# Performance work log

Hardware: AMD Instinct MI355X
Metric: run time of the kernel (lower is better)

## Reference

```python
import jax, jax.numpy as jnp
import numpy as np

KM_ITERS = 25  # fixed Lloyd iterations (original kmeans_pytorch iterates to tol; fixed count for jit)
EPS = 1e-12    # torch F.normalize clamp_min eps


def l2_normalize(x):
    n = jnp.sqrt(jnp.sum(x * x, axis=1, keepdims=True))
    return x / jnp.maximum(n, EPS)


def kmeans(X, k, iters=KM_ITERS):
    """Lloyd's algorithm, euclidean distance, deterministic init from first k rows."""
    N = X.shape[0]
    centers0 = X[:k]
    xsq = jnp.sum(X * X, axis=1, keepdims=True)  # [N,1]

    def dist2(centers):
        # squared euclidean distances [N,k]; argmin identical to euclidean
        return xsq - 2.0 * (X @ centers.T) + jnp.sum(centers * centers, axis=1)

    def step(i, centers):
        lab = jnp.argmin(dist2(centers), axis=1)  # [N]
        sums = jax.ops.segment_sum(X, lab, num_segments=k)  # [k,d]
        cnts = jax.ops.segment_sum(jnp.ones((N,), X.dtype), lab, num_segments=k)  # [k]
        new = sums / jnp.maximum(cnts, 1.0)[:, None]
        # keep old center for empty clusters
        return jnp.where(cnts[:, None] > 0, new, centers)

    centers = jax.lax.fori_loop(0, iters, step, centers0)
    labels = jnp.argmin(dist2(centers), axis=1)
    return labels, centers


def setup_inputs() -> dict:
    key = jax.random.key(0)
    ks = jax.random.split(key, 8)
    N, D, H, K = 50000, 1024, 512, 64
    x = jax.random.normal(ks[0], (N, D), dtype=jnp.float32)
    xw = jax.random.normal(ks[1], (N, D), dtype=jnp.float32)
    s1 = 1.0 / np.sqrt(D)
    s2 = 1.0 / np.sqrt(H)
    W1 = jax.random.uniform(ks[2], (D, H), jnp.float32, -s1, s1)
    b1 = jax.random.uniform(ks[3], (H,), jnp.float32, -s1, s1)
    W2 = jax.random.uniform(ks[4], (D, H), jnp.float32, -s1, s1)
    b2 = jax.random.uniform(ks[5], (H,), jnp.float32, -s1, s1)
    Wc = jax.random.uniform(ks[6], (H, K), jnp.float32, -s2, s2)
    bc = jax.random.uniform(ks[7], (K,), jnp.float32, -s2, s2)
    return {"x": x, "xw": xw, "W1": W1, "b1": b1, "W2": W2, "b2": b2,
            "Wc": Wc, "bc": bc, "n_clusters": K}


def reference(x, xw, W1, b1, W2, b2, Wc, bc, n_clusters):
    out1 = l2_normalize(x @ W1 + b1)   # layers1 + F.normalize(dim=1)
    out2 = l2_normalize(xw @ W2 + b2)  # layers2 + F.normalize(dim=1)
    # kmeans results are detached in the original (converted to numpy)
    km_label, km_centers = kmeans(jax.lax.stop_gradient(out2), n_clusters)
    u1 = jax.nn.softmax(out1 @ Wc + bc, axis=1)
    u2 = jax.nn.softmax(out2 @ Wc + bc, axis=1)
    return (out1, out2, km_label, km_centers, u1, u2)
```

## Files before the change

### kernel.cpp

```cpp
#include <hip/hip_runtime.h>
#include <math.h>

#define ND 1024
#define HID 512
#define KCL 64
#define KM_ITERS 25
#define CHSZ 256


__device__ __forceinline__ float np_pw512_sq(const float* __restrict__ a, int lane)
{
#pragma clang fp contract(off)
  float r = 0.f;
  if (lane < 32) {
    const float* blk = a + 128 * (lane >> 3);
    int j = lane & 7;
    float t = blk[j];
    r = t * t;
#pragma unroll
    for (int i = 8; i < 128; i += 8) { float u = blk[j + i]; r = r + u * u; }
  }
  float t1 = r  + __shfl_xor(r,  1);
  float t2 = t1 + __shfl_xor(t1, 2);
  float t3 = t2 + __shfl_xor(t2, 4);
  float u4 = t3 + __shfl_xor(t3, 8);
  float v5 = u4 + __shfl_xor(u4, 16);
  return __shfl(v5, 0);
}

__global__ __launch_bounds__(512) void np_gemm2_kernel(
    const float* __restrict__ A, const float* __restrict__ W,
    const float* __restrict__ bias, float* __restrict__ C)
{
#pragma clang fp contract(off)
  const int t = threadIdx.x;
  const size_t r0 = (size_t)blockIdx.x * 8;
  const float* a0p = A + r0 * ND;
  float s1[8], s2[8], s3[8], s4[8];
#pragma unroll
  for (int r = 0; r < 8; r++) { s1[r] = 0.f; s2[r] = 0.f; s3[r] = 0.f; s4[r] = 0.f; }

#define G2_STEP(ACC, K4)                                                       \
  {                                                                            \
    const int k = (K4) * 4;                                                    \
    float w0 = W[(size_t)(k + 0) * HID + t];                                   \
    float w1 = W[(size_t)(k + 1) * HID + t];                                   \
    float w2 = W[(size_t)(k + 2) * HID + t];                                   \
    float w3 = W[(size_t)(k + 3) * HID + t];                                   \
    _Pragma("unroll")                                                          \
    for (int r = 0; r < 8; r++) {                                              \
      float4 a = *reinterpret_cast<const float4*>(a0p + (size_t)r * ND + k);   \
      float s = ACC[r];                                                        \
      s = fmaf(a.x, w0, s);                                                    \
      s = fmaf(a.y, w1, s);                                                    \
      s = fmaf(a.z, w2, s);                                                    \
      s = fmaf(a.w, w3, s);                                                    \
      ACC[r] = s;                                                              \
    }                                                                          \
  }

#pragma unroll 2
  for (int k4 = 0; k4 < 80; k4++)    G2_STEP(s1, k4)
#pragma unroll 2
  for (int k4 = 80; k4 < 160; k4++)  G2_STEP(s2, k4)
#pragma unroll 2
  for (int k4 = 160; k4 < 208; k4++) G2_STEP(s3, k4)
#pragma unroll 2
  for (int k4 = 208; k4 < 256; k4++) G2_STEP(s4, k4)
#undef G2_STEP

  float b = bias[t];
#pragma unroll
  for (int r = 0; r < 8; r++)
    C[(r0 + r) * HID + t] = (((s1[r] + s2[r]) + s3[r]) + s4[r]) + b;
}

__global__ __launch_bounds__(256) void np_rownorm_xsq_kernel(
    float* __restrict__ M, float* __restrict__ xsq, int N)
{
#pragma clang fp contract(off)
  __shared__ float sy[4][512];
  int w = threadIdx.x >> 6, lane = threadIdx.x & 63;
  int r = blockIdx.x * 4 + w;
  if (r >= N) return;
  float* row = M + (size_t)r * HID;
  float s = np_pw512_sq(row, lane);
  float n = fmaxf((float)sqrt((double)s), 1e-12f);
#pragma unroll
  for (int j = 0; j < 8; j++) {
    float y = row[lane * 8 + j] / n;
    row[lane * 8 + j] = y;
    sy[w][lane * 8 + j] = y;
  }
  __syncthreads();
  float s2 = np_pw512_sq(sy[w], lane);
  if (lane == 0) xsq[r] = s2;
}

__global__ __launch_bounds__(64) void np_csqT_kernel(
    const float* __restrict__ cen, float* __restrict__ csq, float* __restrict__ Ct)
{
#pragma clang fp contract(off)
  int c = blockIdx.x;
  int lane = threadIdx.x;
  const float* row = cen + (size_t)c * HID;
  float s = np_pw512_sq(row, lane);
  if (lane == 0) csq[c] = s;
  for (int k = lane; k < HID; k += 64) Ct[(size_t)k * KCL + c] = row[k];
}

__global__ __launch_bounds__(256) void np_label_kernel(
    const float* __restrict__ X, const float* __restrict__ Ct,
    const float* __restrict__ xsq, const float* __restrict__ csq,
    int* __restrict__ lab, int N)
{
#pragma clang fp contract(off)
  __shared__ float Xs[16][512];
  const int t = threadIdx.x;
  const int p0 = blockIdx.x * 16;
  const float4* Xg = (const float4*)(X + (size_t)p0 * HID);
  float4* Xs4 = (float4*)&Xs[0][0];
  for (int i = t; i < 16 * 128; i += 256) Xs4[i] = Xg[i];
  __syncthreads();

  const int w = t >> 6, c = t & 63;
  const int pl = w * 4;
  float s0[4], s1[4];
#pragma unroll
  for (int pt = 0; pt < 4; pt++) { s0[pt] = 0.f; s1[pt] = 0.f; }

#pragma unroll 8
  for (int k = 0; k < 256; k++) {
    float ct = Ct[(size_t)k * KCL + c];
#pragma unroll
    for (int pt = 0; pt < 4; pt++) s0[pt] = fmaf(Xs[pl + pt][k], ct, s0[pt]);
  }
#pragma unroll 8
  for (int k = 256; k < 512; k++) {
    float ct = Ct[(size_t)k * KCL + c];
#pragma unroll
    for (int pt = 0; pt < 4; pt++) s1[pt] = fmaf(Xs[pl + pt][k], ct, s1[pt]);
  }

#pragma unroll
  for (int pt = 0; pt < 4; pt++) {
    int p = p0 + pl + pt;
    float dot = s0[pt] + s1[pt];
    float t2 = 2.0f * dot;
    float u = xsq[p] - t2;
    float sc = u + csq[c];
    float bv = sc; int bi = c;
#pragma unroll
    for (int m = 32; m; m >>= 1) {
      float ov = __shfl_xor(bv, m);
      int   oi = __shfl_xor(bi, m);
      if (ov < bv || (ov == bv && oi < bi)) { bv = ov; bi = oi; }
    }
    if (c == 0 && p < N) lab[p] = bi;
  }
}


__global__ __launch_bounds__(256) void k_count(
    const int* __restrict__ lab, int* __restrict__ cntch, int N)
{
  int ch = blockIdx.x;
  int p = ch * CHSZ + threadIdx.x;
  int l = (p < N) ? lab[p] : -1;
  int w = threadIdx.x >> 6, lane = threadIdx.x & 63;
  __shared__ int wc[4][64];
  for (int cc = 0; cc < 64; cc++) {
    unsigned long long mm = __ballot(l == cc);
    if (lane == cc) wc[w][cc] = __popcll(mm);
  }
  __syncthreads();
  if (threadIdx.x < 64) {
    int cc = threadIdx.x;
    cntch[ch * 64 + cc] = wc[0][cc] + wc[1][cc] + wc[2][cc] + wc[3][cc];
  }
}

__global__ __launch_bounds__(64) void k_prefix(
    const int* __restrict__ cntch, int* __restrict__ off,
    int* __restrict__ base, int* __restrict__ cnt, int CH)
{
  int c = threadIdx.x;
  int run = 0;
  for (int ch = 0; ch < CH; ch++) { off[ch * 64 + c] = run; run += cntch[ch * 64 + c]; }
  cnt[c] = run;
  __shared__ int tot[64];
  tot[c] = run;
  __syncthreads();
  if (c == 0) {
    int b = 0;
    for (int cc = 0; cc < 64; cc++) { base[cc] = b; b += tot[cc]; }
  }
  __syncthreads();
  int b = base[c];
  for (int ch = 0; ch < CH; ch++) off[ch * 64 + c] += b;
}

__global__ __launch_bounds__(256) void k_scatter(
    const int* __restrict__ lab, const int* __restrict__ off,
    int* __restrict__ list, int N)
{
  int ch = blockIdx.x;
  int p = ch * CHSZ + threadIdx.x;
  int l = (p < N) ? lab[p] : -1;
  int w = threadIdx.x >> 6, lane = threadIdx.x & 63;
  __shared__ int wc[4][64];
  int rank = 0;
  for (int cc = 0; cc < 64; cc++) {
    unsigned long long mm = __ballot(l == cc);
    if (lane == cc) wc[w][cc] = __popcll(mm);
    if (l == cc) rank = __popcll(mm & ((1ull << lane) - 1ull));
  }
  __syncthreads();
  if (p < N) {
    int before = 0;
    for (int ww = 0; ww < 4; ww++) if (ww < w) before += wc[ww][l];
    list[off[ch * 64 + l] + before + rank] = p;
  }
}

__global__ __launch_bounds__(256) void np_seg_kernel(
    const float* __restrict__ X, const int* __restrict__ list,
    const int* __restrict__ base, const int* __restrict__ cnt,
    float* __restrict__ sums)
{
#pragma clang fp contract(off)
  const int c = blockIdx.x;
  const int d = blockIdx.y * 256 + threadIdx.x;
  const int n = cnt[c];
  const int* lp = list + base[c];
  float s = 0.f;
  int i = 0;
  for (; i + 8 <= n; i += 8) {
    int p0 = lp[i + 0], p1 = lp[i + 1], p2 = lp[i + 2], p3 = lp[i + 3];
    int p4 = lp[i + 4], p5 = lp[i + 5], p6 = lp[i + 6], p7 = lp[i + 7];
    float x0 = X[(size_t)p0 * HID + d];
    float x1 = X[(size_t)p1 * HID + d];
    float x2 = X[(size_t)p2 * HID + d];
    float x3 = X[(size_t)p3 * HID + d];
    float x4 = X[(size_t)p4 * HID + d];
    float x5 = X[(size_t)p5 * HID + d];
    float x6 = X[(size_t)p6 * HID + d];
    float x7 = X[(size_t)p7 * HID + d];
    s = s + x0; s = s + x1; s = s + x2; s = s + x3;
    s = s + x4; s = s + x5; s = s + x6; s = s + x7;
  }
  for (; i < n; i++) s = s + X[(size_t)lp[i] * HID + d];
  sums[(size_t)c * HID + d] = s;
}

__global__ __launch_bounds__(512) void np_update_csqT_kernel(
    const float* __restrict__ sums, const int* __restrict__ cnt,
    float* __restrict__ cen, float* __restrict__ csq, float* __restrict__ Ct)
{
#pragma clang fp contract(off)
  __shared__ float row[512];
  const int c = blockIdx.x, d = threadIdx.x;
  const int n = cnt[c];
  float v;
  if (n > 0) {
    v = sums[(size_t)c * HID + d] / fmaxf((float)n, 1.0f);
    cen[(size_t)c * HID + d] = v;
  } else {
    v = cen[(size_t)c * HID + d];
  }
  row[d] = v;
  __syncthreads();
  if (d < 64) {
    float s = np_pw512_sq(row, d);
    if (d == 0) csq[c] = s;
  }
  Ct[(size_t)d * KCL + c] = v;
}

__global__ void copy_f32_kernel(const float* __restrict__ s, float* __restrict__ d, int n)
{
  int i = blockIdx.x * blockDim.x + threadIdx.x;
  if (i < n) d[i] = s[i];
}
__global__ void lab_to_f32_kernel(const int* __restrict__ s, float* __restrict__ d, int n)
{
  int i = blockIdx.x * blockDim.x + threadIdx.x;
  if (i < n) d[i] = (float)s[i];
}


__global__ __launch_bounds__(256) void rownorm_kernel(float* __restrict__ M, int N)
{
  int r = blockIdx.x * 4 + (threadIdx.x >> 6);
  int lane = threadIdx.x & 63;
  if (r >= N) return;
  float* row = M + (size_t)r * HID;
  float4 v0 = *reinterpret_cast<const float4*>(&row[lane * 8]);
  float4 v1 = *reinterpret_cast<const float4*>(&row[lane * 8 + 4]);
  float s = v0.x*v0.x + v0.y*v0.y + v0.z*v0.z + v0.w*v0.w
          + v1.x*v1.x + v1.y*v1.y + v1.z*v1.z + v1.w*v1.w;
#pragma unroll
  for (int off = 32; off; off >>= 1) s += __shfl_xor(s, off);
  float nrm = fmaxf(sqrtf(s), 1e-12f);
  v0.x /= nrm; v0.y /= nrm; v0.z /= nrm; v0.w /= nrm;
  v1.x /= nrm; v1.y /= nrm; v1.z /= nrm; v1.w /= nrm;
  *reinterpret_cast<float4*>(&row[lane * 8]) = v0;
  *reinterpret_cast<float4*>(&row[lane * 8 + 4]) = v1;
}

__global__ __launch_bounds__(256) void clf_softmax_kernel(
    const float* __restrict__ X, const float* __restrict__ W,
    const float* __restrict__ bias, float* __restrict__ U, int N)
{
  int p = blockIdx.x * 4 + (threadIdx.x >> 6);
  int c = threadIdx.x & 63;
  if (p >= N) return;
  const float* xr = X + (size_t)p * HID;
  float acc = 0.f;
  for (int d = 0; d < HID; d++) acc = fmaf(xr[d], W[(size_t)d * KCL + c], acc);
  float l = acc + bias[c];
  float mx = l;
#pragma unroll
  for (int m = 32; m; m >>= 1) mx = fmaxf(mx, __shfl_xor(mx, m));
  float e = expf(l - mx);
  float s = e;
#pragma unroll
  for (int m = 32; m; m >>= 1) s += __shfl_xor(s, m);
  U[(size_t)p * KCL + c] = e / s;
}

extern "C" void kernel_launch(void* const* d_in, const int* in_sizes, int n_in,
                              void* d_out, int out_size, void* d_ws, size_t ws_size,
                              hipStream_t stream)
{
  const float* x  = (const float*)d_in[0];
  const float* xw = (const float*)d_in[1];
  const float* W1 = (const float*)d_in[2];
  const float* b1 = (const float*)d_in[3];
  const float* W2 = (const float*)d_in[4];
  const float* b2 = (const float*)d_in[5];
  const float* Wc = (const float*)d_in[6];
  const float* bc = (const float*)d_in[7];

  const int N = in_sizes[0] / ND;
  float* out  = (float*)d_out;
  float* out1 = out;
  float* out2 = out1 + (size_t)N * HID;
  float* labf = out2 + (size_t)N * HID;
  float* cenf = labf + N;
  float* u1   = cenf + (size_t)KCL * HID;
  float* u2   = u1 + (size_t)N * KCL;

  const int CH = (N + CHSZ - 1) / CHSZ;

  float* cen   = u2;
  float* Ct    = cen + KCL * HID;
  float* csq   = Ct + KCL * HID;
  float* sums  = csq + KCL;
  float* xsq   = sums + KCL * HID;
  int*   cnt   = (int*)(xsq + N);
  int*   lab   = cnt + KCL;
  int*   list  = lab + N;
  int*   cntch = list + N;
  int*   off   = cntch + CH * 64;
  int*   base  = off + CH * 64;

  const int pblocks = (N + 3) / 4;
  const int lblocks = (N + 15) / 16;

  np_gemm2_kernel<<<N / 8, 512, 0, stream>>>(xw, W2, b2, out2);
  np_rownorm_xsq_kernel<<<pblocks, 256, 0, stream>>>(out2, xsq, N);
  copy_f32_kernel<<<(KCL * HID + 255) / 256, 256, 0, stream>>>(out2, cen, KCL * HID);
  np_csqT_kernel<<<KCL, 64, 0, stream>>>(cen, csq, Ct);

  for (int it = 0; it < KM_ITERS; ++it) {
    np_label_kernel<<<lblocks, 256, 0, stream>>>(out2, Ct, xsq, csq, lab, N);
    k_count<<<CH, 256, 0, stream>>>(lab, cntch, N);
    k_prefix<<<1, 64, 0, stream>>>(cntch, off, base, cnt, CH);
    k_scatter<<<CH, 256, 0, stream>>>(lab, off, list, N);
    np_seg_kernel<<<dim3(KCL, 2), 256, 0, stream>>>(out2, list, base, cnt, sums);
    np_update_csqT_kernel<<<KCL, 512, 0, stream>>>(sums, cnt, cen, csq, Ct);
  }
  np_label_kernel<<<lblocks, 256, 0, stream>>>(out2, Ct, xsq, csq, lab, N);

  lab_to_f32_kernel<<<(N + 255) / 256, 256, 0, stream>>>(lab, labf, N);
  copy_f32_kernel<<<(KCL * HID + 255) / 256, 256, 0, stream>>>(cen, cenf, KCL * HID);

  np_gemm2_kernel<<<N / 8, 512, 0, stream>>>(x, W1, b1, out1);
  rownorm_kernel<<<pblocks, 256, 0, stream>>>(out1, N);
  clf_softmax_kernel<<<pblocks, 256, 0, stream>>>(out1, Wc, bc, u1, N);
  clf_softmax_kernel<<<pblocks, 256, 0, stream>>>(out2, Wc, bc, u2, N);
}
```

Measured before the change: 8.521 ms.

## Stage GEMM rows in LDS, vectorize label dot products, fuse segment-sum with center update

The GEMM kernel now processes 16 rows per block and stages them in shared memory, so each W column load is reused across twice as many rows. The label kernel stores transposed centers in float4-interleaved layout and reads both X and centers as float4. The segment-sum and center-update kernels are merged into one 512-thread kernel per cluster, dropping the sums buffer and one launch per iteration, and the prefix loops get unroll pragmas. Risks include lower occupancy from 64 KB of LDS and 64 accumulators per thread in the GEMM, and only 64 blocks for the fused segment kernel.

Measured after the change: 8.693 ms. +2.0%, slower.

```diff
diff --git a/kernel.cpp b/kernel.cpp
--- a/kernel.cpp
+++ b/kernel.cpp
@@ -33,30 +33,34 @@
     const float* __restrict__ bias, float* __restrict__ C)
 {
 #pragma clang fp contract(off)
+  __shared__ float4 As4[16 * 256];
   const int t = threadIdx.x;
-  const size_t r0 = (size_t)blockIdx.x * 8;
-  const float* a0p = A + r0 * ND;
-  float s1[8], s2[8], s3[8], s4[8];
-#pragma unroll
-  for (int r = 0; r < 8; r++) { s1[r] = 0.f; s2[r] = 0.f; s3[r] = 0.f; s4[r] = 0.f; }
-
-#define G2_STEP(ACC, K4)                                                       \
-  {                                                                            \
-    const int k = (K4) * 4;                                                    \
-    float w0 = W[(size_t)(k + 0) * HID + t];                                   \
-    float w1 = W[(size_t)(k + 1) * HID + t];                                   \
-    float w2 = W[(size_t)(k + 2) * HID + t];                                   \
-    float w3 = W[(size_t)(k + 3) * HID + t];                                   \
-    _Pragma("unroll")                                                          \
-    for (int r = 0; r < 8; r++) {                                              \
-      float4 a = *reinterpret_cast<const float4*>(a0p + (size_t)r * ND + k);   \
-      float s = ACC[r];                                                        \
-      s = fmaf(a.x, w0, s);                                                    \
-      s = fmaf(a.y, w1, s);                                                    \
-      s = fmaf(a.z, w2, s);                                                    \
-      s = fmaf(a.w, w3, s);                                                    \
-      ACC[r] = s;                                                              \
-    }                                                                          \
+  const size_t r0 = (size_t)blockIdx.x * 16;
+  const float4* Ag = (const float4*)(A + r0 * ND);
+  for (int i = t; i < 16 * 256; i += 512) As4[i] = Ag[i];
+  __syncthreads();
+
+  float s1[16], s2[16], s3[16], s4[16];
+#pragma unroll
+  for (int r = 0; r < 16; r++) { s1[r] = 0.f; s2[r] = 0.f; s3[r] = 0.f; s4[r] = 0.f; }
+
+#define G2_STEP(ACC, K4)                                          \
+  {                                                               \
+    const int k = (K4) * 4;                                       \
+    float w0 = W[(size_t)(k + 0) * HID + t];                      \
+    float w1 = W[(size_t)(k + 1) * HID + t];                      \
+    float w2 = W[(size_t)(k + 2) * HID + t];                      \
+    float w3 = W[(size_t)(k + 3) * HID + t];                      \
+    _Pragma("unroll")                                             \
+    for (int r = 0; r < 16; r++) {                                \
+      float4 a = As4[r * 256 + (K4)];                             \
+      float s = ACC[r];                                           \
+      s = fmaf(a.x, w0, s);                                       \
+      s = fmaf(a.y, w1, s);                                       \
+      s = fmaf(a.z, w2, s);                                       \
+      s = fmaf(a.w, w3, s);                                       \
+      ACC[r] = s;                                                 \
+    }                                                             \
   }
 
 #pragma unroll 2
@@ -71,7 +75,7 @@
 
   float b = bias[t];
 #pragma unroll
-  for (int r = 0; r < 8; r++)
+  for (int r = 0; r < 16; r++)
     C[(r0 + r) * HID + t] = (((s1[r] + s2[r]) + s3[r]) + s4[r]) + b;
 }
 
@@ -98,7 +102,7 @@
 }
 
 __global__ __launch_bounds__(64) void np_csqT_kernel(
-    const float* __restrict__ cen, float* __restrict__ csq, float* __restrict__ Ct)
+    const float* __restrict__ cen, float* __restrict__ csq, float* __restrict__ Ct4f)
 {
 #pragma clang fp contract(off)
   int c = blockIdx.x;
@@ -106,45 +110,61 @@
   const float* row = cen + (size_t)c * HID;
   float s = np_pw512_sq(row, lane);
   if (lane == 0) csq[c] = s;
-  for (int k = lane; k < HID; k += 64) Ct[(size_t)k * KCL + c] = row[k];
+  for (int k = lane; k < HID; k += 64)
+    Ct4f[((size_t)(k >> 2) * KCL + c) * 4 + (k & 3)] = row[k];
 }
 
 __global__ __launch_bounds__(256) void np_label_kernel(
-    const float* __restrict__ X, const float* __restrict__ Ct,
+    const float* __restrict__ X, const float4* __restrict__ Ct4,
     const float* __restrict__ xsq, const float* __restrict__ csq,
     int* __restrict__ lab, int N)
 {
 #pragma clang fp contract(off)
-  __shared__ float Xs[16][512];
+  __shared__ float4 Xs4[16 * 128];
   const int t = threadIdx.x;
   const int p0 = blockIdx.x * 16;
   const float4* Xg = (const float4*)(X + (size_t)p0 * HID);
-  float4* Xs4 = (float4*)&Xs[0][0];
   for (int i = t; i < 16 * 128; i += 256) Xs4[i] = Xg[i];
   __syncthreads();
 
   const int w = t >> 6, c = t & 63;
-  const int pl = w * 4;
+  const int pb = w * 4 * 128;
   float s0[4], s1[4];
 #pragma unroll
   for (int pt = 0; pt < 4; pt++) { s0[pt] = 0.f; s1[pt] = 0.f; }
 
-#pragma unroll 8
-  for (int k = 0; k < 256; k++) {
-    float ct = Ct[(size_t)k * KCL + c];
-#pragma unroll
-    for (int pt = 0; pt < 4; pt++) s0[pt] = fmaf(Xs[pl + pt][k], ct, s0[pt]);
-  }
-#pragma unroll 8
-  for (int k = 256; k < 512; k++) {
-    float ct = Ct[(size_t)k * KCL + c];
-#pragma unroll
-    for (int pt = 0; pt < 4; pt++) s1[pt] = fmaf(Xs[pl + pt][k], ct, s1[pt]);
+#pragma unroll 4
+  for (int k4 = 0; k4 < 64; k4++) {
+    float4 ct = Ct4[(size_t)k4 * KCL + c];
+#pragma unroll
+    for (int pt = 0; pt < 4; pt++) {
+      float4 xq = Xs4[pb + pt * 128 + k4];
+      float s = s0[pt];
+      s = fmaf(xq.x, ct.x, s);
+      s = fmaf(xq.y, ct.y, s);
+      s = fmaf(xq.z, ct.z, s);
+      s = fmaf(xq.w, ct.w, s);
+      s0[pt] = s;
+    }
+  }
+#pragma unroll 4
+  for (int k4 = 64; k4 < 128; k4++) {
+    float4 ct = Ct4[(size_t)k4 * KCL + c];
+#pragma unroll
+    for (int pt = 0; pt < 4; pt++) {
+      float4 xq = Xs4[pb + pt * 128 + k4];
+      float s = s1[pt];
+      s = fmaf(xq.x, ct.x, s);
+      s = fmaf(xq.y, ct.y, s);
+      s = fmaf(xq.z, ct.z, s);
+      s = fmaf(xq.w, ct.w, s);
+      s1[pt] = s;
+    }
   }
 
 #pragma unroll
   for (int pt = 0; pt < 4; pt++) {
-    int p = p0 + pl + pt;
+    int p = p0 + (w * 4 + pt);
     float dot = s0[pt] + s1[pt];
     float t2 = 2.0f * dot;
     float u = xsq[p] - t2;
@@ -186,6 +206,7 @@
 {
   int c = threadIdx.x;
   int run = 0;
+#pragma unroll 8
   for (int ch = 0; ch < CH; ch++) { off[ch * 64 + c] = run; run += cntch[ch * 64 + c]; }
   cnt[c] = run;
   __shared__ int tot[64];
@@ -197,6 +218,7 @@
   }
   __syncthreads();
   int b = base[c];
+#pragma unroll 8
   for (int ch = 0; ch < CH; ch++) off[ch * 64 + c] += b;
 }
 
@@ -223,14 +245,15 @@
   }
 }
 
-__global__ __launch_bounds__(256) void np_seg_kernel(
+__global__ __launch_bounds__(512) void np_seg_update_kernel(
     const float* __restrict__ X, const int* __restrict__ list,
     const int* __restrict__ base, const int* __restrict__ cnt,
-    float* __restrict__ sums)
-{
-#pragma clang fp contract(off)
+    float* __restrict__ cen, float* __restrict__ csq, float* __restrict__ Ct4f)
+{
+#pragma clang fp contract(off)
+  __shared__ float row[512];
   const int c = blockIdx.x;
-  const int d = blockIdx.y * 256 + threadIdx.x;
+  const int d = threadIdx.x;
   const int n = cnt[c];
   const int* lp = list + base[c];
   float s = 0.f;
@@ -250,20 +273,10 @@
     s = s + x4; s = s + x5; s = s + x6; s = s + x7;
   }
   for (; i < n; i++) s = s + X[(size_t)lp[i] * HID + d];
-  sums[(size_t)c * HID + d] = s;
-}
-
-__global__ __launch_bounds__(512) void np_update_csqT_kernel(
-    const float* __restrict__ sums, const int* __restrict__ cnt,
-    float* __restrict__ cen, float* __restrict__ csq, float* __restrict__ Ct)
-{
-#pragma clang fp contract(off)
-  __shared__ float row[512];
-  const int c = blockIdx.x, d = threadIdx.x;
-  const int n = cnt[c];
+
   float v;
   if (n > 0) {
-    v = sums[(size_t)c * HID + d] / fmaxf((float)n, 1.0f);
+    v = s / fmaxf((float)n, 1.0f);
     cen[(size_t)c * HID + d] = v;
   } else {
     v = cen[(size_t)c * HID + d];
@@ -271,10 +284,10 @@
   row[d] = v;
   __syncthreads();
   if (d < 64) {
-    float s = np_pw512_sq(row, d);
-    if (d == 0) csq[c] = s;
-  }
-  Ct[(size_t)d * KCL + c] = v;
+    float sq = np_pw512_sq(row, d);
+    if (d == 0) csq[c] = sq;
+  }
+  Ct4f[((size_t)(d >> 2) * KCL + c) * 4 + (d & 3)] = v;
 }
 
 __global__ void copy_f32_kernel(const float* __restrict__ s, float* __restrict__ d, int n)
@@ -354,39 +367,39 @@
   const int CH = (N + CHSZ - 1) / CHSZ;
 
   float* cen   = u2;
-  float* Ct    = cen + KCL * HID;
-  float* csq   = Ct + KCL * HID;
-  float* sums  = csq + KCL;
-  float* xsq   = sums + KCL * HID;
+  float* Ct4f  = cen + KCL * HID;
+  float* csq   = Ct4f + 128 * KCL * 4;
+  float* xsq   = csq + KCL;
   int*   cnt   = (int*)(xsq + N);
   int*   lab   = cnt + KCL;
   int*   list  = lab + N;
   int*   cntch = list + N;
   int*   off   = cntch + CH * 64;
   int*   base  = off + CH * 64;
+  const float4* Ct4 = (const float4*)Ct4f;
 
   const int pblocks = (N + 3) / 4;
+  const int gblocks = N / 16;
   const int lblocks = (N + 15) / 16;
 
-  np_gemm2_kernel<<<N / 8, 512, 0, stream>>>(xw, W2, b2, out2);
+  np_gemm2_kernel<<<gblocks, 512, 0, stream>>>(xw, W2, b2, out2);
   np_rownorm_xsq_kernel<<<pblocks, 256, 0, stream>>>(out2, xsq, N);
   copy_f32_kernel<<<(KCL * HID + 255) / 256, 256, 0, stream>>>(out2, cen, KCL * HID);
-  np_csqT_kernel<<<KCL, 64, 0, stream>>>(cen, csq, Ct);
+  np_csqT_kernel<<<KCL, 64, 0, stream>>>(cen, csq, Ct4f);
 
   for (int it = 0; it < KM_ITERS; ++it) {
-    np_label_kernel<<<lblocks, 256, 0, stream>>>(out2, Ct, xsq, csq, lab, N);
+    np_label_kernel<<<lblocks, 256, 0, stream>>>(out2, Ct4, xsq, csq, lab, N);
     k_count<<<CH, 256, 0, stream>>>(lab, cntch, N);
     k_prefix<<<1, 64, 0, stream>>>(cntch, off, base, cnt, CH);
     k_scatter<<<CH, 256, 0, stream>>>(lab, off, list, N);
-    np_seg_kernel<<<dim3(KCL, 2), 256, 0, stream>>>(out2, list, base, cnt, sums);
-    np_update_csqT_kernel<<<KCL, 512, 0, stream>>>(sums, cnt, cen, csq, Ct);
-  }
-  np_label_kernel<<<lblocks, 256, 0, stream>>>(out2, Ct, xsq, csq, lab, N);
+    np_seg_update_kernel<<<KCL, 512, 0, stream>>>(out2, list, base, cnt, cen, csq, Ct4f);
+  }
+  np_label_kernel<<<lblocks, 256, 0, stream>>>(out2, Ct4, xsq, csq, lab, N);
 
   lab_to_f32_kernel<<<(N + 255) / 256, 256, 0, stream>>>(lab, labf, N);
   copy_f32_kernel<<<(KCL * HID + 255) / 256, 256, 0, stream>>>(cen, cenf, KCL * HID);
 
-  np_gemm2_kernel<<<N / 8, 512, 0, stream>>>(x, W1, b1, out1);
+  np_gemm2_kernel<<<gblocks, 512, 0, stream>>>(x, W1, b1, out1);
   rownorm_kernel<<<pblocks, 256, 0, stream>>>(out1, N);
   clf_softmax_kernel<<<pblocks, 256, 0, stream>>>(out1, Wc, bc, u1, N);
   clf_softmax_kernel<<<pblocks, 256, 0, stream>>>(out2, Wc, bc, u2, N);
```
